# Optimization experiments

Measured on AMD Instinct MI355X. Metric: run time of the kernel, lower is better.

The kernel has to match this reference:

```python
import jax, jax.numpy as jnp
import numpy as np

N_HEADS = 16


def _rope(x, sin, cos):
    # x: [B, H, T, D]; sin/cos: [1, 1, T, D]
    x1 = x[..., ::2]
    x2 = x[..., 1::2]
    xr = jnp.stack((-x2, x1), axis=-1).reshape(x.shape)
    return x * cos + xr * sin


def setup_inputs() -> dict:
    key = jax.random.key(0)
    k_x, k_s, k_c, k_w1, k_w2 = jax.random.split(key, 5)
    B, T, C = 4, 2048, 2048
    hd = C // N_HEADS
    x = jax.random.normal(k_x, (B, T, C), dtype=jnp.float32)
    sin = jax.random.uniform(k_s, (1, 1, T, hd), dtype=jnp.float32)
    cos = jax.random.uniform(k_c, (1, 1, T, hd), dtype=jnp.float32)
    W_qkv = jax.random.normal(k_w1, (C, 3 * C), dtype=jnp.float32) * 0.02
    W_proj = jax.random.normal(k_w2, (C, C), dtype=jnp.float32) * 0.02
    return {"x": x, "sin": sin, "cos": cos, "W_qkv": W_qkv, "W_proj": W_proj}


def reference(x, sin, cos, W_qkv, W_proj):
    B, T, C = x.shape
    hd = C // N_HEADS
    qkv = x @ W_qkv  # [B, T, 3C]
    q, k, v = jnp.split(qkv, 3, axis=-1)
    # [B, T, C] -> [B, H, T, D]
    q = q.reshape(B, T, N_HEADS, hd).transpose(0, 2, 1, 3)
    k = k.reshape(B, T, N_HEADS, hd).transpose(0, 2, 1, 3)
    v = v.reshape(B, T, N_HEADS, hd).transpose(0, 2, 1, 3)
    q = _rope(q, sin[:, :, :T, :], cos[:, :, :T, :])
    k = _rope(k, sin[:, :, :T, :], cos[:, :, :T, :])
    scale = 1.0 / jnp.sqrt(jnp.asarray(hd, dtype=x.dtype))
    scores = jnp.einsum("bhqd,bhkd->bhqk", q, k) * scale
    causal = jnp.tril(jnp.ones((T, T), dtype=bool))
    scores = jnp.where(causal, scores, jnp.asarray(-jnp.inf, dtype=scores.dtype))
    attn = jax.nn.softmax(scores, axis=-1)
    y = jnp.einsum("bhqk,bhkd->bhqd", attn, v)  # [B, H, T, D]
    y = y.transpose(0, 2, 1, 3).reshape(B, T, C)
    return y @ W_proj
```

## Files before the change

kernel.cpp:

```cpp
#include <hip/hip_runtime.h>
#include <hip/hip_bf16.h>
#include <stdint.h>

typedef uint32_t u32;
typedef uint16_t u16;
typedef __attribute__((ext_vector_type(8))) short short8;
typedef __attribute__((ext_vector_type(4))) float floatx4;

#define NH 16
#define HD 128
#define TSEQ 2048
#define NB 4
#define CM 2048
#define MROWS (NB*TSEQ)
#define NQKV (3*CM)

__device__ __forceinline__ u16 f2bf(float f) {
    union { float f; u32 u; } v; v.f = f;
    return (u16)((v.u + 0x7fffu + ((v.u >> 16) & 1u)) >> 16);
}

__global__ __launch_bounds__(256) void convert_x_kernel(const float* __restrict__ in,
                                                        u16* __restrict__ out) {
    int idx = (blockIdx.x * 256 + threadIdx.x) * 8;
    float4 a = *(const float4*)(in + idx);
    float4 b = *(const float4*)(in + idx + 4);
    union { u16 s[8]; uint4 v; } o;
    o.s[0] = f2bf(a.x); o.s[1] = f2bf(a.y); o.s[2] = f2bf(a.z); o.s[3] = f2bf(a.w);
    o.s[4] = f2bf(b.x); o.s[5] = f2bf(b.y); o.s[6] = f2bf(b.z); o.s[7] = f2bf(b.w);
    *(uint4*)(out + idx) = o.v;
}

__global__ __launch_bounds__(256) void transpose_bf_kernel(const float* __restrict__ in,
                                                           u16* __restrict__ out,
                                                           int R, int Cn) {
    __shared__ float tile[32][33];
    int tx = threadIdx.x, ty = threadIdx.y;
    int c0 = blockIdx.x * 32, r0 = blockIdx.y * 32;
#pragma unroll
    for (int i = 0; i < 4; i++)
        tile[ty + i * 8][tx] = in[(size_t)(r0 + ty + i * 8) * Cn + c0 + tx];
    __syncthreads();
#pragma unroll
    for (int i = 0; i < 4; i++)
        out[(size_t)(c0 + ty + i * 8) * R + r0 + tx] = f2bf(tile[tx][ty + i * 8]);
}

__global__ __launch_bounds__(256, 2) void gemm_qkv_rope(const u16* __restrict__ A,
                                                        const u16* __restrict__ BT,
                                                        const float* __restrict__ sinp,
                                                        const float* __restrict__ cosp,
                                                        u16* __restrict__ q_ws,
                                                        u16* __restrict__ k_ws,
                                                        u16* __restrict__ v_ws) {
    __shared__ u16 As[128 * 40];
    __shared__ u16 Bs[128 * 40];
    int tid = threadIdx.x;
    int w = tid >> 6, lane = tid & 63, quad = lane >> 4, l15 = lane & 15;
    int mw = (w >> 1) * 64, nw = (w & 1) * 64;
    int blk = blockIdx.x;
    int xcd = blk & 7, idx8 = blk >> 3;
    int rowBase = (xcd * 8 + (idx8 & 7)) * 128;
    int colBase = (idx8 >> 3) * 128;

    floatx4 acc[4][4];
#pragma unroll
    for (int mi = 0; mi < 4; mi++)
#pragma unroll
        for (int ni = 0; ni < 4; ni++) acc[mi][ni] = (floatx4){0.f, 0.f, 0.f, 0.f};

    int r0s = tid >> 2, c8s = (tid & 3) * 8;
    int r1s = (tid + 256) >> 2;
    const u16* Arow0 = A + (size_t)(rowBase + r0s) * CM + c8s;
    const u16* Arow1 = A + (size_t)(rowBase + r1s) * CM + c8s;
    const u16* Brow0 = BT + (size_t)(colBase + r0s) * CM + c8s;
    const u16* Brow1 = BT + (size_t)(colBase + r1s) * CM + c8s;

    uint4 pa0 = *(const uint4*)(Arow0), pa1 = *(const uint4*)(Arow1);
    uint4 pb0 = *(const uint4*)(Brow0), pb1 = *(const uint4*)(Brow1);

    for (int k0 = 0; k0 < CM; k0 += 32) {
        __syncthreads();
        *(uint4*)(&As[r0s * 40 + c8s]) = pa0;
        *(uint4*)(&As[r1s * 40 + c8s]) = pa1;
        *(uint4*)(&Bs[r0s * 40 + c8s]) = pb0;
        *(uint4*)(&Bs[r1s * 40 + c8s]) = pb1;
        if (k0 + 32 < CM) {
            pa0 = *(const uint4*)(Arow0 + k0 + 32);
            pa1 = *(const uint4*)(Arow1 + k0 + 32);
            pb0 = *(const uint4*)(Brow0 + k0 + 32);
            pb1 = *(const uint4*)(Brow1 + k0 + 32);
        }
        __syncthreads();
        short8 af[4], bf[4];
#pragma unroll
        for (int mi = 0; mi < 4; mi++)
            af[mi] = *(const short8*)(&As[(mw + mi * 16 + l15) * 40 + quad * 8]);
#pragma unroll
        for (int ni = 0; ni < 4; ni++)
            bf[ni] = *(const short8*)(&Bs[(nw + ni * 16 + l15) * 40 + quad * 8]);
#pragma unroll
        for (int mi = 0; mi < 4; mi++)
#pragma unroll
            for (int ni = 0; ni < 4; ni++)
                acc[mi][ni] = __builtin_amdgcn_mfma_f32_16x16x32_bf16(af[mi], bf[ni],
                                                                      acc[mi][ni], 0, 0, 0);
    }

    const float inv_sqrt_hd = 0.08838834764831845f;
#pragma unroll
    for (int mi = 0; mi < 4; mi++) {
#pragma unroll
        for (int ni = 0; ni < 4; ni++) {
            int j = colBase + nw + ni * 16 + l15;
            int sec = j >> 11;
            int jj = j & 2047;
            int h = jj >> 7, d = jj & 127;
            if (sec == 2) {
                int r0 = rowBase + mw + mi * 16 + quad * 4;
                int b = r0 >> 11, t0 = r0 & 2047;
                union { u16 s[4]; uint2 v; } pk;
#pragma unroll
                for (int reg = 0; reg < 4; reg++) pk.s[reg] = f2bf(acc[mi][ni][reg]);
                *(uint2*)(&v_ws[((size_t)(b * NH + h) * HD + d) * TSEQ + t0]) = pk.v;
            } else {
#pragma unroll
                for (int reg = 0; reg < 4; reg++) {
                    int r = rowBase + mw + mi * 16 + quad * 4 + reg;
                    int b = r >> 11, t = r & 2047;
                    float v = acc[mi][ni][reg];
                    float partner = __shfl_xor(v, 1, 64);
                    size_t dsti = (size_t)((b * NH + h) * TSEQ + t) * HD + d;
                    float s = sinp[t * HD + d], c = cosp[t * HD + d];
                    float o = v * c + ((d & 1) ? partner * s : -partner * s);
                    if (sec == 0) o *= inv_sqrt_hd;
                    ((sec == 0) ? q_ws : k_ws)[dsti] = f2bf(o);
                }
            }
        }
    }
}

__global__ __launch_bounds__(256, 2) void attn_kernel(const u16* __restrict__ q_ws,
                                                      const u16* __restrict__ k_ws,
                                                      const u16* __restrict__ vt_ws,
                                                      u16* __restrict__ y_bf) {
    __shared__ u16 Ks[16 * 512];
    __shared__ u16 Vt[8 * 1024];
    __shared__ u16 Ps[128 * 72];
    int tid = threadIdx.x;
    int w = tid >> 6, lane = tid & 63, quad = lane >> 4, l15 = lane & 15;
    int qt = 15 - (blockIdx.x >> 6);
    int bh = blockIdx.x & 63;
    int b = bh >> 4, h = bh & 15;
    const u16* Qg = q_ws + (size_t)bh * TSEQ * HD;
    const u16* Kg = k_ws + (size_t)bh * TSEQ * HD;
    const u16* Vg = vt_ws + (size_t)bh * HD * TSEQ;

    short8 qf[2][4];
#pragma unroll
    for (int mi = 0; mi < 2; mi++)
#pragma unroll
        for (int kk = 0; kk < 4; kk++)
            qf[mi][kk] = *(const short8*)(&Qg[(size_t)(qt * 128 + w * 32 + mi * 16 + l15) * HD +
                                              kk * 32 + quad * 8]);

    floatx4 O[2][8];
#pragma unroll
    for (int mi = 0; mi < 2; mi++)
#pragma unroll
        for (int f = 0; f < 8; f++) O[mi][f] = (floatx4){0.f, 0.f, 0.f, 0.f};
    float l_i[2][4];
#pragma unroll
    for (int mi = 0; mi < 2; mi++)
#pragma unroll
        for (int g = 0; g < 4; g++) l_i[mi][g] = 0.f;

    uint4 kreg[4], vreg[4];
#pragma unroll
    for (int j = 0; j < 4; j++) {
        int s = 4 * w + j;
        kreg[j] = *(const uint4*)(Kg + (size_t)lane * HD + s * 8);
    }
#pragma unroll
    for (int j = 0; j < 4; j++) {
        int s = 2 * w + (j >> 1), hh = j & 1;
        vreg[j] = *(const uint4*)(Vg + (size_t)(hh * 64 + lane) * TSEQ + s * 8);
    }

    int ktmax = 2 * qt + 1;
    for (int kt = 0; kt <= ktmax; kt++) {
        __syncthreads();
#pragma unroll
        for (int j = 0; j < 4; j++) {
            int s = 4 * w + j;
            *(uint4*)(&Ks[s * 512 + lane * 8]) = kreg[j];
        }
#pragma unroll
        for (int j = 0; j < 4; j++) {
            int s = 2 * w + (j >> 1), hh = j & 1;
            *(uint4*)(&Vt[s * 1024 + hh * 512 + lane * 8]) = vreg[j];
        }
        if (kt < ktmax) {
            const u16* Ktg = Kg + (size_t)((kt + 1) * 64) * HD;
            const u16* Vtg = Vg + (kt + 1) * 64;
#pragma unroll
            for (int j = 0; j < 4; j++) {
                int s = 4 * w + j;
                kreg[j] = *(const uint4*)(Ktg + (size_t)lane * HD + s * 8);
            }
#pragma unroll
            for (int j = 0; j < 4; j++) {
                int s = 2 * w + (j >> 1), hh = j & 1;
                vreg[j] = *(const uint4*)(Vtg + (size_t)(hh * 64 + lane) * TSEQ + s * 8);
            }
        }
        __syncthreads();

        floatx4 S[2][4];
#pragma unroll
        for (int nf = 0; nf < 4; nf++) {
            short8 bb[4];
#pragma unroll
            for (int kk = 0; kk < 4; kk++)
                bb[kk] = *(const short8*)(&Ks[(kk * 4 + quad) * 512 + (nf * 16 + l15) * 8]);
#pragma unroll
            for (int mi = 0; mi < 2; mi++) {
                floatx4 a4 = (floatx4){0.f, 0.f, 0.f, 0.f};
#pragma unroll
                for (int kk = 0; kk < 4; kk++)
                    a4 = __builtin_amdgcn_mfma_f32_16x16x32_bf16(qf[mi][kk], bb[kk], a4, 0, 0, 0);
                S[mi][nf] = a4;
            }
        }
        if (kt >= 2 * qt) {
#pragma unroll
            for (int mi = 0; mi < 2; mi++)
#pragma unroll
                for (int nf = 0; nf < 4; nf++) {
                    int key = kt * 64 + nf * 16 + l15;
#pragma unroll
                    for (int reg = 0; reg < 4; reg++) {
                        int query = qt * 128 + w * 32 + mi * 16 + quad * 4 + reg;
                        if (key > query) S[mi][nf][reg] = -1e4f;
                    }
                }
        }
#pragma unroll
        for (int mi = 0; mi < 2; mi++)
#pragma unroll
            for (int nf = 0; nf < 4; nf++)
#pragma unroll
                for (int reg = 0; reg < 4; reg++) {
                    float p = __expf(S[mi][nf][reg]);
                    l_i[mi][reg] += p;
                    Ps[(w * 32 + mi * 16 + quad * 4 + reg) * 72 + nf * 16 + l15] = f2bf(p);
                }
        short8 pa[2][2];
#pragma unroll
        for (int mi = 0; mi < 2; mi++)
#pragma unroll
            for (int kk = 0; kk < 2; kk++)
                pa[mi][kk] = *(const short8*)(&Ps[(w * 32 + mi * 16 + l15) * 72 +
                                                  kk * 32 + quad * 8]);
#pragma unroll
        for (int f = 0; f < 8; f++) {
            short8 vb[2];
#pragma unroll
            for (int kk = 0; kk < 2; kk++)
                vb[kk] = *(const short8*)(&Vt[(kk * 4 + quad) * 1024 + (f * 16 + l15) * 8]);
#pragma unroll
            for (int mi = 0; mi < 2; mi++)
#pragma unroll
                for (int kk = 0; kk < 2; kk++)
                    O[mi][f] = __builtin_amdgcn_mfma_f32_16x16x32_bf16(pa[mi][kk], vb[kk],
                                                                       O[mi][f], 0, 0, 0);
        }
    }

    float inv[2][4];
#pragma unroll
    for (int mi = 0; mi < 2; mi++)
#pragma unroll
        for (int reg = 0; reg < 4; reg++) {
            float l = l_i[mi][reg];
#pragma unroll
            for (int off = 1; off < 16; off <<= 1) l += __shfl_xor(l, off, 64);
            inv[mi][reg] = 1.0f / l;
        }
#pragma unroll
    for (int mi = 0; mi < 2; mi++)
#pragma unroll
        for (int f = 0; f < 8; f++)
#pragma unroll
            for (int reg = 0; reg < 4; reg++) {
                int t = qt * 128 + w * 32 + mi * 16 + quad * 4 + reg;
                int col = h * HD + f * 16 + l15;
                y_bf[(size_t)(b * TSEQ + t) * CM + col] = f2bf(O[mi][f][reg] * inv[mi][reg]);
            }
}

__global__ __launch_bounds__(256, 2) void gemm_proj(const u16* __restrict__ A,
                                                    const u16* __restrict__ BT,
                                                    float* __restrict__ out) {
    __shared__ u16 As[128 * 40];
    __shared__ u16 Bs[128 * 40];
    int tid = threadIdx.x;
    int w = tid >> 6, lane = tid & 63, quad = lane >> 4, l15 = lane & 15;
    int mw = (w >> 1) * 64, nw = (w & 1) * 64;
    int blk = blockIdx.x;
    int xcd = blk & 7, idx8 = blk >> 3;
    int rowBase = (xcd * 8 + (idx8 & 7)) * 128;
    int colBase = (idx8 >> 3) * 128;

    floatx4 acc[4][4];
#pragma unroll
    for (int mi = 0; mi < 4; mi++)
#pragma unroll
        for (int ni = 0; ni < 4; ni++) acc[mi][ni] = (floatx4){0.f, 0.f, 0.f, 0.f};

    int r0s = tid >> 2, c8s = (tid & 3) * 8;
    int r1s = (tid + 256) >> 2;
    const u16* Arow0 = A + (size_t)(rowBase + r0s) * CM + c8s;
    const u16* Arow1 = A + (size_t)(rowBase + r1s) * CM + c8s;
    const u16* Brow0 = BT + (size_t)(colBase + r0s) * CM + c8s;
    const u16* Brow1 = BT + (size_t)(colBase + r1s) * CM + c8s;

    uint4 pa0 = *(const uint4*)(Arow0), pa1 = *(const uint4*)(Arow1);
    uint4 pb0 = *(const uint4*)(Brow0), pb1 = *(const uint4*)(Brow1);

    for (int k0 = 0; k0 < CM; k0 += 32) {
        __syncthreads();
        *(uint4*)(&As[r0s * 40 + c8s]) = pa0;
        *(uint4*)(&As[r1s * 40 + c8s]) = pa1;
        *(uint4*)(&Bs[r0s * 40 + c8s]) = pb0;
        *(uint4*)(&Bs[r1s * 40 + c8s]) = pb1;
        if (k0 + 32 < CM) {
            pa0 = *(const uint4*)(Arow0 + k0 + 32);
            pa1 = *(const uint4*)(Arow1 + k0 + 32);
            pb0 = *(const uint4*)(Brow0 + k0 + 32);
            pb1 = *(const uint4*)(Brow1 + k0 + 32);
        }
        __syncthreads();
        short8 af[4], bf[4];
#pragma unroll
        for (int mi = 0; mi < 4; mi++)
            af[mi] = *(const short8*)(&As[(mw + mi * 16 + l15) * 40 + quad * 8]);
#pragma unroll
        for (int ni = 0; ni < 4; ni++)
            bf[ni] = *(const short8*)(&Bs[(nw + ni * 16 + l15) * 40 + quad * 8]);
#pragma unroll
        for (int mi = 0; mi < 4; mi++)
#pragma unroll
            for (int ni = 0; ni < 4; ni++)
                acc[mi][ni] = __builtin_amdgcn_mfma_f32_16x16x32_bf16(af[mi], bf[ni],
                                                                      acc[mi][ni], 0, 0, 0);
    }

#pragma unroll
    for (int mi = 0; mi < 4; mi++) {
#pragma unroll
        for (int ni = 0; ni < 4; ni++) {
            int j = colBase + nw + ni * 16 + l15;
#pragma unroll
            for (int reg = 0; reg < 4; reg++) {
                int r = rowBase + mw + mi * 16 + quad * 4 + reg;
                out[(size_t)r * CM + j] = acc[mi][ni][reg];
            }
        }
    }
}

extern "C" void kernel_launch(void* const* d_in, const int* in_sizes, int n_in,
                              void* d_out, int out_size, void* d_ws, size_t ws_size,
                              hipStream_t stream) {
    const float* x      = (const float*)d_in[0];
    const float* sinp   = (const float*)d_in[1];
    const float* cosp   = (const float*)d_in[2];
    const float* W_qkv  = (const float*)d_in[3];
    const float* W_proj = (const float*)d_in[4];
    float* out = (float*)d_out;

    char* ws = (char*)d_ws;
    size_t off = 0;
    u16* x_bf   = (u16*)(ws + off); off += (size_t)MROWS * CM * 2;
    u16* wqkvT  = (u16*)(ws + off); off += (size_t)NQKV * CM * 2;
    u16* wprojT = (u16*)(ws + off); off += (size_t)CM * CM * 2;
    u16* q_ws   = (u16*)(ws + off); off += (size_t)MROWS * CM * 2;
    u16* k_ws   = (u16*)(ws + off); off += (size_t)MROWS * CM * 2;
    u16* v_ws   = (u16*)(ws + off); off += (size_t)MROWS * CM * 2;
    u16* y_bf   = x_bf;

    convert_x_kernel<<<(MROWS * CM) / (256 * 8), 256, 0, stream>>>(x, x_bf);
    transpose_bf_kernel<<<dim3(NQKV / 32, CM / 32), dim3(32, 8), 0, stream>>>(W_qkv, wqkvT, CM, NQKV);
    transpose_bf_kernel<<<dim3(CM / 32, CM / 32), dim3(32, 8), 0, stream>>>(W_proj, wprojT, CM, CM);
    gemm_qkv_rope<<<(NQKV / 128) * (MROWS / 128), 256, 0, stream>>>(x_bf, wqkvT, sinp, cosp,
                                                                    q_ws, k_ws, v_ws);
    attn_kernel<<<(TSEQ / 128) * 64, 256, 0, stream>>>(q_ws, k_ws, v_ws, y_bf);
    gemm_proj<<<(CM / 128) * (MROWS / 128), 256, 0, stream>>>(y_bf, wprojT, out);
}
```

Measured before the change: 741.5 us.

## Swizzle attention K/V/Q shared layouts, coalesce loads, raise occupancy, move prefetch after barrier

```diff
diff --git a/kernel.cpp b/kernel.cpp
--- a/kernel.cpp
+++ b/kernel.cpp
@@ -85,13 +85,13 @@
         *(uint4*)(&As[r1s * 40 + c8s]) = pa1;
         *(uint4*)(&Bs[r0s * 40 + c8s]) = pb0;
         *(uint4*)(&Bs[r1s * 40 + c8s]) = pb1;
+        __syncthreads();
         if (k0 + 32 < CM) {
             pa0 = *(const uint4*)(Arow0 + k0 + 32);
             pa1 = *(const uint4*)(Arow1 + k0 + 32);
             pb0 = *(const uint4*)(Brow0 + k0 + 32);
             pb1 = *(const uint4*)(Brow1 + k0 + 32);
         }
-        __syncthreads();
         short8 af[4], bf[4];
 #pragma unroll
         for (int mi = 0; mi < 4; mi++)
@@ -141,13 +141,14 @@
     }
 }
 
-__global__ __launch_bounds__(256, 2) void attn_kernel(const u16* __restrict__ q_ws,
+__global__ __launch_bounds__(256, 3) void attn_kernel(const u16* __restrict__ q_ws,
                                                       const u16* __restrict__ k_ws,
                                                       const u16* __restrict__ vt_ws,
                                                       u16* __restrict__ y_bf) {
-    __shared__ u16 Ks[16 * 512];
-    __shared__ u16 Vt[8 * 1024];
+    __shared__ u16 smem[16 * 1024];
     __shared__ u16 Ps[128 * 72];
+    u16* Ks = smem;
+    u16* Vt = smem + 8192;
     int tid = threadIdx.x;
     int w = tid >> 6, lane = tid & 63, quad = lane >> 4, l15 = lane & 15;
     int qt = 15 - (blockIdx.x >> 6);
@@ -157,13 +158,37 @@
     const u16* Kg = k_ws + (size_t)bh * TSEQ * HD;
     const u16* Vg = vt_ws + (size_t)bh * HD * TSEQ;
 
+    uint4 kreg[4], vreg[4];
+#pragma unroll
+    for (int j = 0; j < 4; j++) {
+        int idx = j * 256 + tid;
+        int key = idx >> 4, s = idx & 15;
+        kreg[j] = *(const uint4*)(Kg + (size_t)key * HD + s * 8);
+    }
+#pragma unroll
+    for (int j = 0; j < 4; j++) {
+        int idx = j * 256 + tid;
+        int d = idx >> 3, s = idx & 7;
+        vreg[j] = *(const uint4*)(Vg + (size_t)d * TSEQ + s * 8);
+    }
+
+#pragma unroll
+    for (int j = 0; j < 8; j++) {
+        int idx = j * 256 + tid;
+        int row = idx >> 4, s = idx & 15;
+        uint4 qv = *(const uint4*)(Qg + (size_t)(qt * 128 + row) * HD + s * 8);
+        *(uint4*)(&smem[s * 1024 + ((row ^ (s & 7)) * 8)]) = qv;
+    }
+    __syncthreads();
     short8 qf[2][4];
 #pragma unroll
     for (int mi = 0; mi < 2; mi++)
 #pragma unroll
-        for (int kk = 0; kk < 4; kk++)
-            qf[mi][kk] = *(const short8*)(&Qg[(size_t)(qt * 128 + w * 32 + mi * 16 + l15) * HD +
-                                              kk * 32 + quad * 8]);
+        for (int kk = 0; kk < 4; kk++) {
+            int row = w * 32 + mi * 16 + l15;
+            int s = kk * 4 + quad;
+            qf[mi][kk] = *(const short8*)(&smem[s * 1024 + ((row ^ (s & 7)) * 8)]);
+        }
 
     floatx4 O[2][8];
 #pragma unroll
@@ -176,54 +201,49 @@
 #pragma unroll
         for (int g = 0; g < 4; g++) l_i[mi][g] = 0.f;
 
-    uint4 kreg[4], vreg[4];
-#pragma unroll
-    for (int j = 0; j < 4; j++) {
-        int s = 4 * w + j;
-        kreg[j] = *(const uint4*)(Kg + (size_t)lane * HD + s * 8);
-    }
-#pragma unroll
-    for (int j = 0; j < 4; j++) {
-        int s = 2 * w + (j >> 1), hh = j & 1;
-        vreg[j] = *(const uint4*)(Vg + (size_t)(hh * 64 + lane) * TSEQ + s * 8);
-    }
-
     int ktmax = 2 * qt + 1;
     for (int kt = 0; kt <= ktmax; kt++) {
         __syncthreads();
 #pragma unroll
         for (int j = 0; j < 4; j++) {
-            int s = 4 * w + j;
-            *(uint4*)(&Ks[s * 512 + lane * 8]) = kreg[j];
+            int idx = j * 256 + tid;
+            int key = idx >> 4, s = idx & 15;
+            *(uint4*)(&Ks[s * 512 + ((key ^ (s & 7)) * 8)]) = kreg[j];
         }
 #pragma unroll
         for (int j = 0; j < 4; j++) {
-            int s = 2 * w + (j >> 1), hh = j & 1;
-            *(uint4*)(&Vt[s * 1024 + hh * 512 + lane * 8]) = vreg[j];
-        }
+            int idx = j * 256 + tid;
+            int d = idx >> 3, s = idx & 7;
+            *(uint4*)(&Vt[s * 1024 + ((d ^ s) * 8)]) = vreg[j];
+        }
+        __syncthreads();
         if (kt < ktmax) {
             const u16* Ktg = Kg + (size_t)((kt + 1) * 64) * HD;
             const u16* Vtg = Vg + (kt + 1) * 64;
 #pragma unroll
             for (int j = 0; j < 4; j++) {
-                int s = 4 * w + j;
-                kreg[j] = *(const uint4*)(Ktg + (size_t)lane * HD + s * 8);
+                int idx = j * 256 + tid;
+                int key = idx >> 4, s = idx & 15;
+                kreg[j] = *(const uint4*)(Ktg + (size_t)key * HD + s * 8);
             }
 #pragma unroll
             for (int j = 0; j < 4; j++) {
-                int s = 2 * w + (j >> 1), hh = j & 1;
-                vreg[j] = *(const uint4*)(Vtg + (size_t)(hh * 64 + lane) * TSEQ + s * 8);
-            }
-        }
-        __syncthreads();
+                int idx = j * 256 + tid;
+                int d = idx >> 3, s = idx & 7;
+                vreg[j] = *(const uint4*)(Vtg + (size_t)d * TSEQ + s * 8);
+            }
+        }
 
         floatx4 S[2][4];
 #pragma unroll
         for (int nf = 0; nf < 4; nf++) {
             short8 bb[4];
 #pragma unroll
-            for (int kk = 0; kk < 4; kk++)
-                bb[kk] = *(const short8*)(&Ks[(kk * 4 + quad) * 512 + (nf * 16 + l15) * 8]);
+            for (int kk = 0; kk < 4; kk++) {
+                int s = kk * 4 + quad;
+                int key = nf * 16 + l15;
+                bb[kk] = *(const short8*)(&Ks[s * 512 + ((key ^ (s & 7)) * 8)]);
+            }
 #pragma unroll
             for (int mi = 0; mi < 2; mi++) {
                 floatx4 a4 = (floatx4){0.f, 0.f, 0.f, 0.f};
@@ -267,8 +287,11 @@
         for (int f = 0; f < 8; f++) {
             short8 vb[2];
 #pragma unroll
-            for (int kk = 0; kk < 2; kk++)
-                vb[kk] = *(const short8*)(&Vt[(kk * 4 + quad) * 1024 + (f * 16 + l15) * 8]);
+            for (int kk = 0; kk < 2; kk++) {
+                int s = kk * 4 + quad;
+                int d = f * 16 + l15;
+                vb[kk] = *(const short8*)(&Vt[s * 1024 + ((d ^ s) * 8)]);
+            }
 #pragma unroll
             for (int mi = 0; mi < 2; mi++)
 #pragma unroll
@@ -335,13 +358,13 @@
         *(uint4*)(&As[r1s * 40 + c8s]) = pa1;
         *(uint4*)(&Bs[r0s * 40 + c8s]) = pb0;
         *(uint4*)(&Bs[r1s * 40 + c8s]) = pb1;
+        __syncthreads();
         if (k0 + 32 < CM) {
             pa0 = *(const uint4*)(Arow0 + k0 + 32);
             pa1 = *(const uint4*)(Arow1 + k0 + 32);
             pb0 = *(const uint4*)(Brow0 + k0 + 32);
             pb1 = *(const uint4*)(Brow1 + k0 + 32);
         }
-        __syncthreads();
         short8 af[4], bf[4];
 #pragma unroll
         for (int mi = 0; mi < 4; mi++)
```

Measured after the change: 917.8 us. +23.8%, slower.
